# Kernel tuning notes

Measured on AMD Instinct MI355X. Metric: run time of the kernel, lower is better.

Reference implementation:

```python
import jax, jax.numpy as jnp
import numpy as np

E = 4       # num_edge_types
DEPTH = 3   # args.depth (weight_tying=False -> DEPTH message layers)
V = 117     # num_atom_types


def setup_inputs() -> dict:
    key = jax.random.key(0)
    ks = jax.random.split(key, 13)
    mb, atoms, D, M = 1024, 128, 256, 512
    s = 0.05  # weight scale
    return {
        "atom_array": jax.random.randint(ks[0], (mb, atoms), 0, V),
        "adj": jax.random.uniform(ks[1], (mb, E, atoms, atoms), dtype=jnp.float32),
        "embed": jax.random.normal(ks[2], (V, D), jnp.float32) * s,
        "msg_W": jax.random.normal(ks[3], (DEPTH, E * D, D), jnp.float32) * s,
        "msg_b": jnp.zeros((DEPTH, E * D), jnp.float32),
        "W_ih": jax.random.normal(ks[4], (3 * D, D), jnp.float32) * s,
        "b_ih": jnp.zeros((3 * D,), jnp.float32),
        "W_hh": jax.random.normal(ks[5], (3 * D, D), jnp.float32) * s,
        "b_hh": jnp.zeros((3 * D,), jnp.float32),
        "i_W": jax.random.normal(ks[6], (M, 2 * D), jnp.float32) * s,
        "i_b": jnp.zeros((M,), jnp.float32),
        "j_W": jax.random.normal(ks[7], (M, D), jnp.float32) * s,
        "j_b": jnp.zeros((M,), jnp.float32),
    }


def _gru_cell(x, h, W_ih, b_ih, W_hh, b_hh):
    # PyTorch GRUCell math. x: input (message), h: hidden state.
    gi = x @ W_ih.T + b_ih
    gh = h @ W_hh.T + b_hh
    ir, iz, in_ = jnp.split(gi, 3, axis=-1)
    hr, hz, hn = jnp.split(gh, 3, axis=-1)
    r = jax.nn.sigmoid(ir + hr)
    z = jax.nn.sigmoid(iz + hz)
    n = jnp.tanh(in_ + r * hn)
    return (1.0 - z) * n + z * h


def reference(atom_array, adj, embed, msg_W, msg_b, W_ih, b_ih, W_hh, b_hh, i_W, i_b, j_W, j_b):
    mb, atoms = atom_array.shape
    D = embed.shape[1]
    h = embed[atom_array]          # [mb, atoms, D]
    h0 = h
    for step in range(DEPTH):
        # message: Linear(D -> E*D) then per-edge-type adjacency bmm, summed over edge types
        m = h @ msg_W[step].T + msg_b[step]            # [mb, atoms, E*D]
        m = m.reshape(mb, atoms, E, D).transpose(0, 2, 1, 3)  # [mb, E, atoms, D]
        m = jnp.einsum('beij,bejd->bid', adj, m)       # bmm + sum over edge types
        hid = h if step > 0 else jnp.zeros_like(h)     # GRUCell(hidden=None) at step 0
        h = _gru_cell(m, hid, W_ih, b_ih, W_hh, b_hh)  # [mb, atoms, D]
    # gated readout
    gate = jax.nn.sigmoid(jnp.concatenate([h, h0], axis=-1) @ i_W.T + i_b)  # [mb, atoms, M]
    val = h @ j_W.T + j_b                                                    # [mb, atoms, M]
    return jnp.sum(gate * val, axis=1)                                       # [mb, M]
```

## Files before the change

### kernel.cpp

```cpp
#include <hip/hip_runtime.h>
#include <cstdint>
#include <cstddef>

using f32x4 = float __attribute__((ext_vector_type(4)));
using u16x8 = unsigned short __attribute__((ext_vector_type(8)));
using u16x4 = unsigned short __attribute__((ext_vector_type(4)));
typedef _Float16 f16x8 __attribute__((ext_vector_type(8)));

#define DEV static __device__ __forceinline__

DEV unsigned short f2h(float f) {
  _Float16 x = (_Float16)f;
  return __builtin_bit_cast(unsigned short, x);
}
DEV float h2f(unsigned short s) {
  return (float)__builtin_bit_cast(_Float16, s);
}
DEV float sigm(float x) { return 1.f / (1.f + __expf(-x)); }
DEV float tanh_(float x) { return 2.f / (1.f + __expf(-2.f * x)) - 1.f; }

#define MFMA_F16(acc, va, vb) \
  acc = __builtin_amdgcn_mfma_f32_16x16x32_f16(va, vb, acc, 0, 0, 0)

constexpr int NB = 1024;
constexpr int AT = 128;
constexpr int DD = 256;
constexpr int MOUT = 512;
constexpr long NR = (long)NB * AT;

#define VWAIT(n) do { asm volatile("s_waitcnt vmcnt(" #n ")" ::: "memory"); \
                      __builtin_amdgcn_sched_barrier(0); } while (0)
#define LWAIT do { asm volatile("s_waitcnt lgkmcnt(0)" ::: "memory"); \
                   __builtin_amdgcn_sched_barrier(0); } while (0)
#define BARR do { __builtin_amdgcn_sched_barrier(0); __builtin_amdgcn_s_barrier(); \
                  __builtin_amdgcn_sched_barrier(0); } while (0)

__global__ __launch_bounds__(256) void k_cvt(const float* __restrict__ src,
                                             unsigned short* __restrict__ dst) {
  long base = ((long)blockIdx.x * 256 + threadIdx.x) * 8;
  f32x4 v0 = *(const f32x4*)(src + base);
  f32x4 v1 = *(const f32x4*)(src + base + 4);
  u16x8 o;
  #pragma unroll
  for (int q = 0; q < 4; ++q) o[q] = f2h(v0[q]);
  #pragma unroll
  for (int q = 0; q < 4; ++q) o[4 + q] = f2h(v1[q]);
  *(u16x8*)(dst + base) = o;
}

__global__ __launch_bounds__(256) void k_cvt5(const float* __restrict__ s0, unsigned short* __restrict__ d0,
                                              const float* __restrict__ s1, unsigned short* __restrict__ d1,
                                              const float* __restrict__ s2, unsigned short* __restrict__ d2,
                                              const float* __restrict__ s3, unsigned short* __restrict__ d3,
                                              const float* __restrict__ s4, unsigned short* __restrict__ d4) {
  int blk = blockIdx.x;
  const float* s; unsigned short* d;
  if (blk < 384)      { s = s0; d = d0; }
  else if (blk < 480) { s = s1; d = d1; blk -= 384; }
  else if (blk < 576) { s = s2; d = d2; blk -= 480; }
  else if (blk < 704) { s = s3; d = d3; blk -= 576; }
  else                { s = s4; d = d4; blk -= 704; }
  long base = ((long)blk * 256 + threadIdx.x) * 8;
  f32x4 v0 = *(const f32x4*)(s + base);
  f32x4 v1 = *(const f32x4*)(s + base + 4);
  u16x8 o;
  #pragma unroll
  for (int q = 0; q < 4; ++q) o[q] = f2h(v0[q]);
  #pragma unroll
  for (int q = 0; q < 4; ++q) o[4 + q] = f2h(v1[q]);
  *(u16x8*)(d + base) = o;
}

__global__ __launch_bounds__(256) void k_gather(const int* __restrict__ atom,
                                                const float* __restrict__ embed,
                                                unsigned short* __restrict__ h,
                                                unsigned short* __restrict__ h0) {
  long idx = (long)blockIdx.x * 256 + threadIdx.x;
  long n = idx >> 6;
  int ch = (int)(idx & 63);
  int a = atom[n];
  f32x4 v = *(const f32x4*)(embed + (size_t)a * DD + ch * 4);
  u16x4 o;
  #pragma unroll
  for (int q = 0; q < 4; ++q) o[q] = f2h(v[q]);
  *(u16x4*)(h  + n * DD + ch * 4) = o;
  *(u16x4*)(h0 + n * DD + ch * 4) = o;
}

#define GEMM_IDS \
  const int tid = threadIdx.x, lane = tid & 63, wave = tid >> 6; \
  const int wr = wave >> 1, wc = wave & 1; \
  const int l15 = lane & 15, lg = lane >> 4; \
  const int sseg = (l15 >> 1) & 3;

#define GLDS(SRC, STRIDE, DST) \
  { \
    _Pragma("unroll") \
    for (int j_ = 0; j_ < 2; ++j_) { \
      const unsigned short* g_ = (SRC) + \
          (size_t)((wave * 2 + j_) * 16 + (lane >> 2)) * (STRIDE) + \
          ((lane & 3) ^ ((lane >> 3) & 3)) * 8; \
      __builtin_amdgcn_global_load_lds( \
          (const __attribute__((address_space(1))) void*)g_, \
          (__attribute__((address_space(3))) void*)&DST[(wave * 2 + j_) * 16][0], \
          16, 0, 0); \
    } \
  }

#define GLDS64(SRC, STRIDE, DST) \
  { \
    const unsigned short* g_ = (SRC) + \
        (size_t)(wave * 16 + (lane >> 2)) * (STRIDE) + \
        ((lane & 3) ^ ((lane >> 3) & 3)) * 8; \
    __builtin_amdgcn_global_load_lds( \
        (const __attribute__((address_space(1))) void*)g_, \
        (__attribute__((address_space(3))) void*)&DST[wave * 16][0], \
        16, 0, 0); \
  }

#define LOAD_A(AH) \
  f16x8 ah[4]; \
  _Pragma("unroll") \
  for (int m_ = 0; m_ < 4; ++m_) \
    ah[m_] = *(const f16x8*)&AH[wr * 64 + m_ * 16 + l15][(lg ^ sseg) * 8];

#define LOAD_B(BH) \
  f16x8 bh[4]; \
  _Pragma("unroll") \
  for (int n_ = 0; n_ < 4; ++n_) \
    bh[n_] = *(const f16x8*)&BH[wc * 64 + n_ * 16 + l15][(lg ^ sseg) * 8];

#define MFMA_TILE(ACC) \
  _Pragma("unroll") \
  for (int m_ = 0; m_ < 4; ++m_) \
    _Pragma("unroll") \
    for (int n_ = 0; n_ < 4; ++n_) \
      MFMA_F16(ACC[m_][n_], ah[m_], bh[n_]);

__global__ __launch_bounds__(256) void k_msgadj(const unsigned short* __restrict__ h,
                                                const unsigned short* __restrict__ W,
                                                const float* __restrict__ bias,
                                                const unsigned short* __restrict__ adjh,
                                                unsigned short* __restrict__ m_out) {
  __shared__ __align__(16) char pool[16384 + 128 * 136 * 2];
  typedef unsigned short row32[32];
  row32* As_[2] = { (row32*)pool,          (row32*)(pool + 16384) };
  row32* Bs_[2] = { (row32*)(pool + 8192), (row32*)(pool + 24576) };
  unsigned short (*PT)[136] = (unsigned short (*)[136])(pool + 16384);
  GEMM_IDS
  const size_t b = blockIdx.x;
  const int d0 = blockIdx.y * 128;
  const unsigned short* hb = h + (size_t)b * 128 * 256;
  const unsigned short* adjb = adjh + (size_t)b * 4 * 128 * 128;
  f32x4 accM[4][4] = {};
  for (int e = 0; e < 4; ++e) {
    f32x4 accP[4][4] = {};
    const unsigned short* We = W + (size_t)(e * 256 + d0) * 256;
    const unsigned short* adje = adjb + (size_t)e * 128 * 128;
    GLDS(hb, 256, As_[0])
    GLDS(We, 256, Bs_[0])
    #pragma unroll
    for (int k0i = 0; k0i < 8; ++k0i) {
      const int cur = k0i & 1;
      if (k0i < 7) {
        row32* an_ = As_[cur ^ 1];
        row32* bn_ = Bs_[cur ^ 1];
        GLDS(hb + (k0i + 1) * 32, 256, an_)
        GLDS(We + (k0i + 1) * 32, 256, bn_)
      } else {
        GLDS(adje + 0 * 32, 128, As_[0])
        GLDS(adje + 1 * 32, 128, Bs_[0])
      }
      VWAIT(4);
      BARR;
      {
        row32* ac_ = As_[cur];
        row32* bc_ = Bs_[cur];
        LOAD_A(ac_)
        LOAD_B(bc_)
        MFMA_TILE(accP)
      }
      BARR;
    }
    #pragma unroll
    for (int m_ = 0; m_ < 4; ++m_) {
      int j0 = wr * 64 + m_ * 16 + lg * 4;
      #pragma unroll
      for (int n_ = 0; n_ < 4; ++n_) {
        int c = wc * 64 + n_ * 16 + l15;
        float bb = bias[e * 256 + d0 + c];
        u16x4 o;
        #pragma unroll
        for (int q = 0; q < 4; ++q) o[q] = f2h(accP[m_][n_][q] + bb);
        *(u16x4*)&PT[c][j0] = o;
      }
    }
    LWAIT;
    BARR;
    #pragma unroll
    for (int kt = 0; kt < 4; ++kt) {
      if (kt == 1) { GLDS(adje + 2 * 32, 128, As_[0]) }
      if (kt == 2) { GLDS(adje + 3 * 32, 128, Bs_[0]) }
      if (kt < 3) { VWAIT(2); } else { VWAIT(0); }
      BARR;
      {
        row32* ac_ = (kt & 1) ? Bs_[0] : As_[0];
        LOAD_A(ac_)
        f16x8 bh[4];
        #pragma unroll
        for (int n_ = 0; n_ < 4; ++n_)
          bh[n_] = *(const f16x8*)&PT[wc * 64 + n_ * 16 + l15][kt * 32 + lg * 8];
        MFMA_TILE(accM)
      }
      BARR;
    }
  }
  #pragma unroll
  for (int m_ = 0; m_ < 4; ++m_) {
    int i0 = wr * 64 + m_ * 16 + lg * 4;
    #pragma unroll
    for (int n_ = 0; n_ < 4; ++n_) {
      int c = d0 + wc * 64 + n_ * 16 + l15;
      #pragma unroll
      for (int q = 0; q < 4; ++q)
        m_out[((size_t)b * 128 + i0 + q) * 256 + c] = f2h(accM[m_][n_][q]);
    }
  }
}

template <bool HAS_H>
__global__ __launch_bounds__(256) void k_grufuse(const unsigned short* __restrict__ m,
                                                 const unsigned short* __restrict__ h,
                                                 const unsigned short* __restrict__ wih,
                                                 const unsigned short* __restrict__ whh,
                                                 const float* __restrict__ b_ih,
                                                 const float* __restrict__ b_hh,
                                                 unsigned short* __restrict__ h_new) {
  __shared__ unsigned short As[2][64][32];
  __shared__ unsigned short Br[2][64][32], Bz[2][64][32], Bn[2][64][32];
  GEMM_IDS
  const size_t b = blockIdx.x;
  const int quad = blockIdx.y;
  const int r0 = (quad >> 2) * 64;
  const int c0 = (quad & 3) * 64;
  const unsigned short* msrc = m + ((size_t)b * 128 + r0) * 256;
  const unsigned short* hsrc = h + ((size_t)b * 128 + r0) * 256;
  constexpr int NKT = HAS_H ? 16 : 8;

  f32x4 accR[2][2] = {}, accZ[2][2] = {}, accI[2][2] = {}, accN[2][2] = {};

  auto stage = [&](int t, int s) {
    const unsigned short* a_ = ((HAS_H && t >= 8) ? hsrc : msrc) + (t & 7) * 32;
    const unsigned short* w_ = (HAS_H && t >= 8) ? whh : wih;
    GLDS64(a_, 256, As[s])
    GLDS64(w_ + (size_t)(c0) * 256 + (t & 7) * 32, 256, Br[s])
    GLDS64(w_ + (size_t)(256 + c0) * 256 + (t & 7) * 32, 256, Bz[s])
    GLDS64(w_ + (size_t)(512 + c0) * 256 + (t & 7) * 32, 256, Bn[s])
  };

  stage(0, 0);
  #pragma unroll
  for (int kt = 0; kt < NKT; ++kt) {
    const int cur = kt & 1;
    if (kt + 1 < NKT) stage(kt + 1, cur ^ 1);
    if (kt + 1 < NKT) { VWAIT(4); } else { VWAIT(0); }
    BARR;
    f16x8 af[2], brf[2], bzf[2], bnf[2];
    #pragma unroll
    for (int m_ = 0; m_ < 2; ++m_)
      af[m_] = *(const f16x8*)&As[cur][wr * 32 + m_ * 16 + l15][(lg ^ sseg) * 8];
    #pragma unroll
    for (int n_ = 0; n_ < 2; ++n_) {
      brf[n_] = *(const f16x8*)&Br[cur][wc * 32 + n_ * 16 + l15][(lg ^ sseg) * 8];
      bzf[n_] = *(const f16x8*)&Bz[cur][wc * 32 + n_ * 16 + l15][(lg ^ sseg) * 8];
      bnf[n_] = *(const f16x8*)&Bn[cur][wc * 32 + n_ * 16 + l15][(lg ^ sseg) * 8];
    }
    #pragma unroll
    for (int m_ = 0; m_ < 2; ++m_)
      #pragma unroll
      for (int n_ = 0; n_ < 2; ++n_) {
        MFMA_F16(accR[m_][n_], af[m_], brf[n_]);
        MFMA_F16(accZ[m_][n_], af[m_], bzf[n_]);
        if (!HAS_H || kt < 8) { MFMA_F16(accI[m_][n_], af[m_], bnf[n_]); }
        else                  { MFMA_F16(accN[m_][n_], af[m_], bnf[n_]); }
      }
    BARR;
  }

  #pragma unroll
  for (int m_ = 0; m_ < 2; ++m_) {
    int rloc = r0 + wr * 32 + m_ * 16 + lg * 4;
    #pragma unroll
    for (int n_ = 0; n_ < 2; ++n_) {
      int c = c0 + wc * 32 + n_ * 16 + l15;
      float br = b_ih[c] + b_hh[c];
      float bz = b_ih[256 + c] + b_hh[256 + c];
      float bin = b_ih[512 + c], bhn = b_hh[512 + c];
      #pragma unroll
      for (int q = 0; q < 4; ++q) {
        size_t row = (size_t)b * 128 + rloc + q;
        float r = sigm(accR[m_][n_][q] + br);
        float z = sigm(accZ[m_][n_][q] + bz);
        float hn = (HAS_H ? accN[m_][n_][q] : 0.f) + bhn;
        float nn = tanh_(accI[m_][n_][q] + bin + r * hn);
        float hv = HAS_H ? h2f(h[row * 256 + c]) : 0.f;
        h_new[row * 256 + c] = f2h((1.f - z) * nn + z * hv);
      }
    }
  }
}

__global__ __launch_bounds__(256) void k_readout(const unsigned short* __restrict__ h,
                                                 const unsigned short* __restrict__ h0,
                                                 const unsigned short* __restrict__ iw,
                                                 const unsigned short* __restrict__ jw,
                                                 const float* __restrict__ ib,
                                                 const float* __restrict__ jb,
                                                 float* __restrict__ out) {
  __shared__ unsigned short As[2][128][32];
  __shared__ unsigned short Bg[2][128][32], Bv[2][128][32];
  __shared__ float red[2][128];
  GEMM_IDS
  const size_t b = blockIdx.x;
  const int c0 = blockIdx.y * 128;
  auto as_src = [&](int t) {
    return (t < 8) ? (h + b * 128 * 256 + t * 32) : (h0 + b * 128 * 256 + (t - 8) * 32);
  };
  f32x4 accG[4][4] = {};
  f32x4 accV[4][4] = {};
  GLDS(as_src(0), 256, As[0])
  GLDS(iw + (size_t)c0 * 512, 512, Bg[0])
  GLDS(jw + (size_t)c0 * 256, 256, Bv[0])
  #pragma unroll
  for (int kt = 0; kt < 16; ++kt) {
    const int cur = kt & 1;
    if (kt + 1 < 16) {
      GLDS(as_src(kt + 1), 256, As[cur ^ 1])
      GLDS(iw + (size_t)c0 * 512 + (kt + 1) * 32, 512, Bg[cur ^ 1])
      if (kt + 1 < 8) GLDS(jw + (size_t)c0 * 256 + (kt + 1) * 32, 256, Bv[cur ^ 1])
    }
    if (kt < 7) { VWAIT(6); } else if (kt < 15) { VWAIT(4); } else { VWAIT(0); }
    BARR;
    LOAD_A(As[cur])
    f16x8 bg[4];
    #pragma unroll
    for (int n_ = 0; n_ < 4; ++n_)
      bg[n_] = *(const f16x8*)&Bg[cur][wc * 64 + n_ * 16 + l15][(lg ^ sseg) * 8];
    #pragma unroll
    for (int m_ = 0; m_ < 4; ++m_)
      #pragma unroll
      for (int n_ = 0; n_ < 4; ++n_)
        MFMA_F16(accG[m_][n_], ah[m_], bg[n_]);
    if (kt < 8) {
      f16x8 bv[4];
      #pragma unroll
      for (int n_ = 0; n_ < 4; ++n_)
        bv[n_] = *(const f16x8*)&Bv[cur][wc * 64 + n_ * 16 + l15][(lg ^ sseg) * 8];
      #pragma unroll
      for (int m_ = 0; m_ < 4; ++m_)
        #pragma unroll
        for (int n_ = 0; n_ < 4; ++n_)
          MFMA_F16(accV[m_][n_], ah[m_], bv[n_]);
    }
    BARR;
  }
  #pragma unroll
  for (int n_ = 0; n_ < 4; ++n_) {
    int c = c0 + wc * 64 + n_ * 16 + l15;
    float gb = ib[c], vb = jb[c];
    float s = 0.f;
    #pragma unroll
    for (int m_ = 0; m_ < 4; ++m_)
      #pragma unroll
      for (int q = 0; q < 4; ++q) {
        float g = sigm(accG[m_][n_][q] + gb);
        float v = accV[m_][n_][q] + vb;
        s += g * v;
      }
    s += __shfl_xor(s, 16);
    s += __shfl_xor(s, 32);
    if (lg == 0) red[wr][wc * 64 + n_ * 16 + l15] = s;
  }
  __syncthreads();
  if (tid < 128) out[b * MOUT + c0 + tid] = red[0][tid] + red[1][tid];
}

extern "C" void kernel_launch(void* const* d_in, const int* in_sizes, int n_in,
                              void* d_out, int out_size, void* d_ws, size_t ws_size,
                              hipStream_t stream) {
  const int*   atom  = (const int*)d_in[0];
  const float* adj   = (const float*)d_in[1];
  const float* embed = (const float*)d_in[2];
  const float* msg_W = (const float*)d_in[3];
  const float* msg_b = (const float*)d_in[4];
  const float* W_ih  = (const float*)d_in[5];
  const float* b_ih  = (const float*)d_in[6];
  const float* W_hh  = (const float*)d_in[7];
  const float* b_hh  = (const float*)d_in[8];
  const float* i_W   = (const float*)d_in[9];
  const float* i_b   = (const float*)d_in[10];
  const float* j_W   = (const float*)d_in[11];
  const float* j_b   = (const float*)d_in[12];
  float* out = (float*)d_out;

  const size_t SZ_H   = (size_t)NR * 256 * 2;
  const size_t SZ_ADJ = (size_t)NB * 4 * 128 * 128 * 2;

  char* p = (char*)d_ws;
  unsigned short* hA   = (unsigned short*)p;  p += SZ_H;
  unsigned short* hB   = (unsigned short*)p;  p += SZ_H;
  unsigned short* h0   = (unsigned short*)p;  p += SZ_H;
  unsigned short* m    = (unsigned short*)p;  p += SZ_H;
  unsigned short* adjh = (unsigned short*)p;  p += SZ_ADJ;
  unsigned short* wmsg = (unsigned short*)p;  p += (size_t)3 * 1024 * 256 * 2;
  unsigned short* wih  = (unsigned short*)p;  p += (size_t)768 * 256 * 2;
  unsigned short* whh  = (unsigned short*)p;  p += (size_t)768 * 256 * 2;
  unsigned short* wiw  = (unsigned short*)p;  p += (size_t)512 * 512 * 2;
  unsigned short* wjw  = (unsigned short*)p;  p += (size_t)512 * 256 * 2;
  if ((size_t)(p - (char*)d_ws) > ws_size) return;

  k_cvt<<<(int)((size_t)NB * 4 * 128 * 128 / 2048), 256, 0, stream>>>(adj, adjh);
  k_cvt5<<<768, 256, 0, stream>>>(msg_W, wmsg, W_ih, wih, W_hh, whh, i_W, wiw, j_W, wjw);

  k_gather<<<(int)(NR * 64 / 256), 256, 0, stream>>>(atom, embed, hA, h0);

  unsigned short* h_cur = hA;
  unsigned short* h_nxt = hB;
  for (int step = 0; step < 3; ++step) {
    k_msgadj<<<dim3(NB, 2), 256, 0, stream>>>(h_cur, wmsg + (size_t)step * 262144,
                                              msg_b + (size_t)step * 1024, adjh, m);
    if (step == 0)
      k_grufuse<false><<<dim3(NB, 8), 256, 0, stream>>>(m, h_cur, wih, whh, b_ih, b_hh, h_nxt);
    else
      k_grufuse<true><<<dim3(NB, 8), 256, 0, stream>>>(m, h_cur, wih, whh, b_ih, b_hh, h_nxt);
    unsigned short* t = h_cur; h_cur = h_nxt; h_nxt = t;
  }

  k_readout<<<dim3(NB, 4), 256, 0, stream>>>(h_cur, h0, wiw, wjw, i_b, j_b, out);
}
```

Measured before the change: 1.219 ms.

## Swizzle workgroups across XCDs and triple-buffer GRU kernel loads

```diff
diff --git a/kernel.cpp b/kernel.cpp
--- a/kernel.cpp
+++ b/kernel.cpp
@@ -34,6 +34,8 @@
                    __builtin_amdgcn_sched_barrier(0); } while (0)
 #define BARR do { __builtin_amdgcn_sched_barrier(0); __builtin_amdgcn_s_barrier(); \
                   __builtin_amdgcn_sched_barrier(0); } while (0)
+
+#define XCD_SWZ(WG, N) const int WG = ((int)blockIdx.x & 7) * ((N) / 8) + ((int)blockIdx.x >> 3);
 
 __global__ __launch_bounds__(256) void k_cvt(const float* __restrict__ src,
                                              unsigned short* __restrict__ dst) {
@@ -148,8 +150,9 @@
   row32* Bs_[2] = { (row32*)(pool + 8192), (row32*)(pool + 24576) };
   unsigned short (*PT)[136] = (unsigned short (*)[136])(pool + 16384);
   GEMM_IDS
-  const size_t b = blockIdx.x;
-  const int d0 = blockIdx.y * 128;
+  XCD_SWZ(wg, 2048)
+  const size_t b = wg >> 1;
+  const int d0 = (wg & 1) * 128;
   const unsigned short* hb = h + (size_t)b * 128 * 256;
   const unsigned short* adjb = adjh + (size_t)b * 4 * 128 * 128;
   f32x4 accM[4][4] = {};
@@ -236,11 +239,12 @@
                                                  const float* __restrict__ b_ih,
                                                  const float* __restrict__ b_hh,
                                                  unsigned short* __restrict__ h_new) {
-  __shared__ unsigned short As[2][64][32];
-  __shared__ unsigned short Br[2][64][32], Bz[2][64][32], Bn[2][64][32];
+  __shared__ unsigned short As[3][64][32];
+  __shared__ unsigned short Br[3][64][32], Bz[3][64][32], Bn[3][64][32];
   GEMM_IDS
-  const size_t b = blockIdx.x;
-  const int quad = blockIdx.y;
+  XCD_SWZ(wg, 8192)
+  const size_t b = wg >> 3;
+  const int quad = wg & 7;
   const int r0 = (quad >> 2) * 64;
   const int c0 = (quad & 3) * 64;
   const unsigned short* msrc = m + ((size_t)b * 128 + r0) * 256;
@@ -259,11 +263,12 @@
   };
 
   stage(0, 0);
+  stage(1, 1);
   #pragma unroll
   for (int kt = 0; kt < NKT; ++kt) {
-    const int cur = kt & 1;
-    if (kt + 1 < NKT) stage(kt + 1, cur ^ 1);
-    if (kt + 1 < NKT) { VWAIT(4); } else { VWAIT(0); }
+    const int cur = kt % 3;
+    if (kt + 2 < NKT) stage(kt + 2, (kt + 2) % 3);
+    if (kt + 2 < NKT) { VWAIT(8); } else if (kt + 2 == NKT) { VWAIT(4); } else { VWAIT(0); }
     BARR;
     f16x8 af[2], brf[2], bzf[2], bnf[2];
     #pragma unroll
@@ -321,8 +326,9 @@
   __shared__ unsigned short Bg[2][128][32], Bv[2][128][32];
   __shared__ float red[2][128];
   GEMM_IDS
-  const size_t b = blockIdx.x;
-  const int c0 = blockIdx.y * 128;
+  XCD_SWZ(wg, 4096)
+  const size_t b = wg >> 2;
+  const int c0 = (wg & 3) * 128;
   auto as_src = [&](int t) {
     return (t < 8) ? (h + b * 128 * 256 + t * 32) : (h0 + b * 128 * 256 + (t - 8) * 32);
   };
@@ -427,14 +433,14 @@
   unsigned short* h_cur = hA;
   unsigned short* h_nxt = hB;
   for (int step = 0; step < 3; ++step) {
-    k_msgadj<<<dim3(NB, 2), 256, 0, stream>>>(h_cur, wmsg + (size_t)step * 262144,
-                                              msg_b + (size_t)step * 1024, adjh, m);
+    k_msgadj<<<2048, 256, 0, stream>>>(h_cur, wmsg + (size_t)step * 262144,
+                                       msg_b + (size_t)step * 1024, adjh, m);
     if (step == 0)
-      k_grufuse<false><<<dim3(NB, 8), 256, 0, stream>>>(m, h_cur, wih, whh, b_ih, b_hh, h_nxt);
+      k_grufuse<false><<<8192, 256, 0, stream>>>(m, h_cur, wih, whh, b_ih, b_hh, h_nxt);
     else
-      k_grufuse<true><<<dim3(NB, 8), 256, 0, stream>>>(m, h_cur, wih, whh, b_ih, b_hh, h_nxt);
+      k_grufuse<true><<<8192, 256, 0, stream>>>(m, h_cur, wih, whh, b_ih, b_hh, h_nxt);
     unsigned short* t = h_cur; h_cur = h_nxt; h_nxt = t;
   }
 
-  k_readout<<<dim3(NB, 4), 256, 0, stream>>>(h_cur, h0, wiw, wjw, i_b, j_b, out);
-}
+  k_readout<<<4096, 256, 0, stream>>>(h_cur, h0, wiw, wjw, i_b, j_b, out);
+}
```

Result: faster. 1.106 ms (-9.2%).
